# Optimization experiments

Measured on AMD Instinct MI355X. Metric: run time of the kernel, lower is better.

Reference implementation:

```python
import jax, jax.numpy as jnp
import numpy as np

H = 32
W = 32
CIN = 64
GR = 4
CC = 6  # channels_count
N = 2


def build_a(h, w):
    # Faithful replication of the torch buffer construction (incl. overlapping
    # writes into channel 0, which accumulate multiple -1 entries per row).
    num = h * w
    a = np.zeros((num, CC, num), np.float32)
    for i in range(num):
        if (i + 1) % w != 0 and i + 1 < num:
            a[i, 0, i] = 1.0
            a[i, 0, i + 1] = -1.0
        if i + w < num:
            a[i, 1, i] = 1.0
            a[i, 1, i + w] = -1.0
        if (i + 2) % w != 0 and (i + 1) % w != 0 and (i + 2 < num):
            a[i, 2, i] = 1.0
            a[i, 2, i + 2] = -1.0
        if i + 2 * w < num:
            a[i, 3, i] = 1.0
            a[i, 3, i + 2 * w] = -1.0
        if i % w != 0 and i + w < num:
            a[i, 0, i] = 1.0
            a[i, 0, i + w - 1] = -1.0
        if (i + 1) % w != 0 and i + w < num:
            a[i, 0, i] = 1.0
            a[i, 0, i + w + 1] = -1.0
    for k in range(CC):
        a[-1, k, -1] = 1.0
    return jnp.asarray(a)


def conv2d(x, w, b, pad):
    y = jax.lax.conv_general_dilated(
        x, w, window_strides=(1, 1), padding=[(pad, pad), (pad, pad)],
        dimension_numbers=('NCHW', 'OIHW', 'NCHW'))
    return y + b[None, :, None, None]


def setup_inputs() -> dict:
    key = jax.random.key(0)
    ks = jax.random.split(key, 20)
    s = 0.05
    d = {
        'x': jax.random.normal(ks[0], (N, CIN, H, W), jnp.float32),
        'a': build_a(H, W),
        # grad branch: conv3x3 CIN->CIN, conv3x3 CIN->CC*GR
        'gw1': jax.random.normal(ks[1], (CIN, CIN, 3, 3), jnp.float32) * s,
        'gb1': jnp.zeros((CIN,), jnp.float32),
        'gw2': jax.random.normal(ks[2], (CC * GR, CIN, 3, 3), jnp.float32) * s,
        'gb2': jnp.zeros((CC * GR,), jnp.float32),
        # att branch (sigmoid at end)
        'aw1': jax.random.normal(ks[3], (CIN, CIN, 3, 3), jnp.float32) * s,
        'ab1': jnp.zeros((CIN,), jnp.float32),
        'aw2': jax.random.normal(ks[4], (CC * GR, CIN, 3, 3), jnp.float32) * s,
        'ab2': jnp.zeros((CC * GR,), jnp.float32),
        # SE branch: 1x1 CIN->CIN//2, 1x1 CIN//2->GR
        'sw1': jax.random.normal(ks[5], (CIN // 2, CIN, 1, 1), jnp.float32) * s,
        'sb1': jnp.zeros((CIN // 2,), jnp.float32),
        'sw2': jax.random.normal(ks[6], (GR, CIN // 2, 1, 1), jnp.float32) * s,
        'sb2': jnp.zeros((GR,), jnp.float32),
        # GroupNorm(1, GR) affine params
        'gn_g': jnp.ones((GR,), jnp.float32),
        'gn_b': jnp.zeros((GR,), jnp.float32),
        # post conv3x3 GR->128
        'pw': jax.random.normal(ks[7], (128, GR, 3, 3), jnp.float32) * s,
        'pb': jnp.zeros((128,), jnp.float32),
    }
    return d


def reference(x, a, gw1, gb1, gw2, gb2, aw1, ab1, aw2, ab2,
              sw1, sb1, sw2, sb2, gn_g, gn_b, pw, pb):
    n, c, h, w = x.shape
    hw = h * w
    lrelu = lambda t: jax.nn.leaky_relu(t, 0.01)

    att = jax.nn.sigmoid(conv2d(lrelu(conv2d(x, aw1, ab1, 1)), aw2, ab2, 1))
    grad = conv2d(lrelu(conv2d(x, gw1, gb1, 1)), gw2, gb2, 1)
    pooled = jnp.mean(x, axis=(2, 3), keepdims=True)
    se = jax.nn.sigmoid(conv2d(lrelu(conv2d(pooled, sw1, sb1, 0)), sw2, sb2, 0))  # [n,GR,1,1]

    b = n * GR
    att = att.reshape(b, CC, hw, 1).transpose(0, 2, 1, 3)   # [b, hw, CC, 1]
    grad = grad.reshape(b, CC, hw, 1).transpose(0, 2, 1, 3)  # [b, hw, CC, 1]

    A = (a[None] * att).reshape(b, hw * CC, hw)   # [b, hw*CC, hw]
    B = (grad * att).reshape(b, hw * CC)          # [b, hw*CC]

    ATA = jnp.einsum('bkm,bkn->bmn', A, A) + 1e-12 * jnp.eye(hw, dtype=x.dtype)
    ATB = jnp.einsum('bkm,bk->bm', A, B)[..., None]
    sol = jnp.linalg.solve(ATA, ATB).reshape(n, GR, h, w)

    # GroupNorm(1, GR): normalize over all (GR,h,w) per sample, per-channel affine
    mu = jnp.mean(sol, axis=(1, 2, 3), keepdims=True)
    var = jnp.var(sol, axis=(1, 2, 3), keepdims=True)
    y = (sol - mu) / jnp.sqrt(var + 1e-5)
    y = y * gn_g[None, :, None, None] + gn_b[None, :, None, None]

    y = se * y
    return conv2d(y, pw, pb, 1)
```

## Files before the change

### kernel.cpp

```cpp
#include <hip/hip_runtime.h>
#include <math.h>

#define HW 1024

__device__ __forceinline__ float lrelu(float v) { return v > 0.f ? v : 0.01f * v; }
__device__ __forceinline__ float sigmoidf(float v) { return 1.f / (1.f + expf(-v)); }

__device__ __forceinline__ float dpp_prev(float x) {
  return __int_as_float(__builtin_amdgcn_update_dpp(
      0, __float_as_int(x), 0x111, 0xF, 0xF, true));
}
__device__ __forceinline__ float dpp_next(float x) {
  return __int_as_float(__builtin_amdgcn_update_dpp(
      0, __float_as_int(x), 0x101, 0xF, 0xF, true));
}

template <int CTRL, int RMASK>
__device__ __forceinline__ float dpp_add(float x) {
  return x + __int_as_float(__builtin_amdgcn_update_dpp(
      0, __float_as_int(x), CTRL, RMASK, 0xF, true));
}
__device__ __forceinline__ float wave_red_bcast(float x) {
  x = dpp_add<0x111, 0xF>(x);
  x = dpp_add<0x112, 0xF>(x);
  x = dpp_add<0x114, 0xF>(x);
  x = dpp_add<0x118, 0xF>(x);
  x = dpp_add<0x142, 0xA>(x);
  x = dpp_add<0x143, 0xC>(x);
  return __int_as_float(__builtin_amdgcn_readlane(__float_as_int(x), 63));
}

__device__ __forceinline__ float frcp(float x) { return __builtin_amdgcn_rcpf(x); }

__device__ __forceinline__ float block_reduce(float v, float* red, int tid) {
#pragma unroll
  for (int off = 32; off > 0; off >>= 1) v += __shfl_xor(v, off, 64);
  if ((tid & 63) == 0) red[tid >> 6] = v;
  __syncthreads();
  float s = red[0] + red[1] + red[2] + red[3];
  __syncthreads();
  return s;
}

template <int MODE>
__device__ __forceinline__ void conv_direct(
    const float* __restrict__ X,
    const float* __restrict__ Wb,
    float bias,
    float* __restrict__ outp,
    int rb) {
  __shared__ float4 sred[192];
  __shared__ float wl[576];
  int tid = threadIdx.x;
  int w = tid >> 6, l = tid & 63;
  int c4 = l & 7, ry = l >> 3;
  int r = rb * 8 + ry;
  int c0 = c4 * 4;
  float lmf = (c4 == 0) ? 0.f : 1.f;
  float rmf = (c4 == 7) ? 0.f : 1.f;
  if (tid < 144) ((float4*)wl)[tid] = ((const float4*)Wb)[tid];
  int rrc[3];
  float rmk[3];
#pragma unroll
  for (int dr = 0; dr < 3; ++dr) {
    int rr = r - 1 + dr;
    bool ok = (unsigned)rr < 32u;
    rrc[dr] = ok ? rr * 32 : 0;
    rmk[dr] = ok ? 1.f : 0.f;
  }
  __syncthreads();
  const float* Xw = X + w * 16 * HW;
  const float* Wp = wl + w * 144;
  float ax = 0.f, ay = 0.f, az = 0.f, aq = 0.f;
#pragma unroll 4
  for (int i = 0; i < 16; ++i) {
    const float* pl = Xw + i * HW;
    const float* wq = Wp + i * 9;
#pragma unroll
    for (int dr = 0; dr < 3; ++dr) {
      const float* rp = pl + rrc[dr];
      float4 m = *(const float4*)(rp + c0);
      float L = dpp_prev(m.w) * lmf;
      float R = dpp_next(m.x) * rmf;
      float w0 = wq[dr * 3 + 0] * rmk[dr];
      float w1 = wq[dr * 3 + 1] * rmk[dr];
      float w2 = wq[dr * 3 + 2] * rmk[dr];
      ax += w0 * L   + w1 * m.x + w2 * m.y;
      ay += w0 * m.x + w1 * m.y + w2 * m.z;
      az += w0 * m.y + w1 * m.z + w2 * m.w;
      aq += w0 * m.z + w1 * m.w + w2 * R;
    }
  }
  __syncthreads();
  if (w > 0) sred[(w - 1) * 64 + l] = make_float4(ax, ay, az, aq);
  __syncthreads();
  if (w == 0) {
    float4 p0 = sred[l], p1 = sred[64 + l], p2 = sred[128 + l];
    float o0 = ax + p0.x + p1.x + p2.x + bias;
    float o1 = ay + p0.y + p1.y + p2.y + bias;
    float o2 = az + p0.z + p1.z + p2.z + bias;
    float o3 = aq + p0.w + p1.w + p2.w + bias;
    if (MODE == 0) { o0 = lrelu(o0); o1 = lrelu(o1); o2 = lrelu(o2); o3 = lrelu(o3); }
    else if (MODE == 1) { o0 = sigmoidf(o0); o1 = sigmoidf(o1); o2 = sigmoidf(o2); o3 = sigmoidf(o3); }
    *(float4*)(outp + r * 32 + c0) = make_float4(o0, o1, o2, o3);
  }
}

__global__ __launch_bounds__(256) void conv64_pool(const float* __restrict__ x,
    const float* __restrict__ aw, const float* __restrict__ ab,
    const float* __restrict__ gw, const float* __restrict__ gb,
    float* __restrict__ t1, float* __restrict__ pooled) {
  int bx = blockIdx.x;
  if (bx < 1024) {
    int co = bx & 63, t = bx >> 6, rb = t & 3, g = t >> 2;
    int br = g >> 1, n = g & 1;
    conv_direct<0>(x + n * 64 * HW,
                   (br ? gw : aw) + co * 576,
                   (br ? gb : ab)[co],
                   t1 + (g * 64 + co) * HW, rb);
  } else {
    __shared__ float red[4];
    int p = bx - 1024;
    const float* px = x + p * HW;
    int tid = threadIdx.x;
    float s = px[tid] + px[tid + 256] + px[tid + 512] + px[tid + 768];
    s = block_reduce(s, red, tid);
    if (tid == 0) pooled[p] = s * (1.f / 1024.f);
  }
}

__global__ __launch_bounds__(256) void conv24_k(const float* __restrict__ t1,
    const float* __restrict__ aw2, const float* __restrict__ ab2,
    const float* __restrict__ gw2, const float* __restrict__ gb2,
    float* __restrict__ attb, float* __restrict__ gradb) {
  int bx = blockIdx.x;
  int co = bx % 24, t = bx / 24, rb = t & 3, g = t >> 2;
  int br = g >> 1, n = g & 1;
  const float* X = t1 + g * 64 * HW;
  const float* Wb = (br ? gw2 : aw2) + co * 576;
  float bias = (br ? gb2 : ab2)[co];
  float* outp = (br ? gradb : attb) + (n * 24 + co) * HW;
  if (br) conv_direct<2>(X, Wb, bias, outp, rb);
  else    conv_direct<1>(X, Wb, bias, outp, rb);
}

__global__ __launch_bounds__(256, 1) void cg_solve(const float* __restrict__ att,
    const float* __restrict__ grad, float* __restrict__ sol,
    int maxit, float tolrel) {
  int b = blockIdx.x, tid = threadIdx.x;
  __shared__ float As[7 * 1088];
  __shared__ __align__(16) float ub0[1152];
  __shared__ __align__(16) float ub1[1152];
  __shared__ __align__(16) float2 redb[2][4];
  float* OD1  = As;
  float* OD2  = As + 1 * 1088;
  float* OD30 = As + 2 * 1088;
  float* OD31 = As + 3 * 1088;
  float* OD32 = As + 4 * 1088;
  float* OD33 = As + 5 * 1088;
  float* OD64 = As + 6 * 1088;
  for (int i = tid; i < 448; i += 256) As[(i >> 6) * 1088 + (i & 63)] = 0.f;
  if (tid < 64) {
    ub0[tid] = 0.f; ub0[1088 + tid] = 0.f;
    ub1[tid] = 0.f; ub1[1088 + tid] = 0.f;
  }

  const float* attb = att + b * 6 * HW;
  const float* grdb = grad + b * 6 * HW;
  const int m0 = 4 * tid;
  const int idx0 = 64 + m0;
  float rk[4], d0v[4], d0r[4];
#pragma unroll
  for (int k = 0; k < 4; ++k) {
    int m = m0 + k;
    int mr = m & 31;
    bool p1 = (mr != 31) && (m < 1023);
    bool p2 = (mr != 0) && (m < 992);
    bool p3 = (mr != 31) && (m < 992);
    bool dd = p1 | p2 | p3;
    bool c1 = m < 992;
    bool c2 = (mr != 30) && (mr != 31) && (m < 1022);
    bool c3 = m < 960;
    float a0 = attb[m],            g0 = grdb[m];
    float a1 = attb[HW + m],       g1 = grdb[HW + m];
    float a2 = attb[2 * HW + m],   g2 = grdb[2 * HW + m];
    float a3 = attb[3 * HW + m],   g3 = grdb[3 * HW + m];
    float u0 = a0 * a0, t0 = u0 * g0;
    float u1 = a1 * a1, t1 = u1 * g1;
    float u2 = a2 * a2, t2 = u2 * g2;
    float u3 = a3 * a3, t3 = u3 * g3;
    float u0m1 = 0.f, t0m1 = 0.f; bool p1m1 = false, p2m1 = false, p3m1 = false;
    if (m >= 1) {
      int j = m - 1; int jr = j & 31;
      p1m1 = (jr != 31) && (j < 1023); p2m1 = (jr != 0) && (j < 992); p3m1 = (jr != 31) && (j < 992);
      float a = attb[j], g = grdb[j]; u0m1 = a * a; t0m1 = u0m1 * g;
    }
    float u0m31 = 0.f, t0m31 = 0.f; bool p2m31 = false, p3m31 = false;
    if (m >= 31) {
      int j = m - 31; int jr = j & 31;
      p2m31 = (jr != 0) && (j < 992); p3m31 = (jr != 31) && (j < 992);
      float a = attb[j], g = grdb[j]; u0m31 = a * a; t0m31 = u0m31 * g;
    }
    float u0m33 = 0.f, t0m33 = 0.f; bool p3m33 = false;
    if (m >= 33) {
      int j = m - 33; int jr = j & 31;
      p3m33 = (jr != 31) && (j < 992);
      float a = attb[j], g = grdb[j]; u0m33 = a * a; t0m33 = u0m33 * g;
    }
    float u1m32 = 0.f, t1m32 = 0.f; bool c1m32 = false;
    if (m >= 32) {
      int j = m - 32; c1m32 = (j < 992);
      float a = attb[HW + j], g = grdb[HW + j]; u1m32 = a * a; t1m32 = u1m32 * g;
    }
    float u2m2 = 0.f, t2m2 = 0.f; bool c2m2 = false;
    if (m >= 2) {
      int j = m - 2; int jr = j & 31;
      c2m2 = (jr != 30) && (jr != 31) && (j < 1022);
      float a = attb[2 * HW + j], g = grdb[2 * HW + j]; u2m2 = a * a; t2m2 = u2m2 * g;
    }
    float u3m64 = 0.f, t3m64 = 0.f; bool c3m64 = false;
    if (m >= 64) {
      int j = m - 64; c3m64 = (j < 960);
      float a = attb[3 * HW + j], g = grdb[3 * HW + j]; u3m64 = a * a; t3m64 = u3m64 * g;
    }
    float d0 = (dd ? u0 : 0.f) + (c1 ? u1 : 0.f) + (c2 ? u2 : 0.f) + (c3 ? u3 : 0.f)
             + (p1m1 ? u0m1 : 0.f) + (p2m31 ? u0m31 : 0.f) + (p3m33 ? u0m33 : 0.f)
             + (c1m32 ? u1m32 : 0.f) + (c2m2 ? u2m2 : 0.f) + (c3m64 ? u3m64 : 0.f) + 1e-12f;
    float rhs = (dd ? t0 : 0.f) + (c1 ? t1 : 0.f) + (c2 ? t2 : 0.f) + (c3 ? t3 : 0.f)
              - (p1m1 ? t0m1 : 0.f) - (p2m31 ? t0m31 : 0.f) - (p3m33 ? t0m33 : 0.f)
              - (c1m32 ? t1m32 : 0.f) - (c2m2 ? t2m2 : 0.f) - (c3m64 ? t3m64 : 0.f);
    if (m == 1023) {
      float a4 = attb[4 * HW + 1023], g4 = grdb[4 * HW + 1023];
      float a5 = attb[5 * HW + 1023], g5 = grdb[5 * HW + 1023];
      d0 += u0 + u1 + u2 + u3 + a4 * a4 + a5 * a5;
      rhs += t0 + t1 + t2 + t3 + a4 * a4 * g4 + a5 * a5 * g5;
    }
    int idx = idx0 + k;
    OD1[idx]  = p1 ? -u0 : 0.f;
    OD31[idx] = p2 ? -u0 : 0.f;
    OD33[idx] = p3 ? -u0 : 0.f;
    OD2[idx]  = (c2 ? -u2 : 0.f) + ((p2m31 && p3m31) ? u0m31 : 0.f);
    OD30[idx] = (p1m1 && p2m1) ? u0m1 : 0.f;
    OD32[idx] = (c1 ? -u1 : 0.f) + ((p1m1 && p3m1) ? u0m1 : 0.f);
    OD64[idx] = c3 ? -u3 : 0.f;
    d0v[k] = d0;
    d0r[k] = 1.f / d0;
    rk[k] = rhs;
  }
  __syncthreads();

  float c1p[4], c1m[4], c2p[4], c2m[4], c30p[4], c30m[4], c31p[4], c31m[4];
  float c32p[4], c32m[4], c33p[4], c33m[4], c64p[4], c64m[4];
#pragma unroll
  for (int k = 0; k < 4; ++k) {
    int idx = idx0 + k;
    c1p[k]  = OD1[idx];  c1m[k]  = OD1[idx - 1];
    c2p[k]  = OD2[idx];  c2m[k]  = OD2[idx - 2];
    c30p[k] = OD30[idx]; c30m[k] = OD30[idx - 30];
    c31p[k] = OD31[idx]; c31m[k] = OD31[idx - 31];
    c32p[k] = OD32[idx]; c32m[k] = OD32[idx - 32];
    c33p[k] = OD33[idx]; c33m[k] = OD33[idx - 33];
    c64p[k] = OD64[idx]; c64m[k] = OD64[idx - 64];
  }

#define SPMV(BASE, UK, NK)                                                   \
  {                                                                          \
    const float* bp = (BASE) + idx0;                                         \
    float2 A01 = *(const float2*)(bp - 2);                                   \
    float2 A67 = *(const float2*)(bp + 4);                                   \
    float2 B01 = *(const float2*)(bp + 30);                                  \
    float4 B25 = *(const float4*)(bp + 32);                                  \
    float  B6  = bp[36];                                                     \
    float  C0  = bp[-33];                                                    \
    float4 C14 = *(const float4*)(bp - 32);                                  \
    float2 C56 = *(const float2*)(bp - 28);                                  \
    float4 Dp  = *(const float4*)(bp + 64);                                  \
    float4 Ep  = *(const float4*)(bp - 64);                                  \
    float Aa[8] = {A01.x, A01.y, UK[0], UK[1], UK[2], UK[3], A67.x, A67.y};  \
    float Ba[7] = {B01.x, B01.y, B25.x, B25.y, B25.z, B25.w, B6};            \
    float Ca[7] = {C0, C14.x, C14.y, C14.z, C14.w, C56.x, C56.y};            \
    float Da[4] = {Dp.x, Dp.y, Dp.z, Dp.w};                                  \
    float Ea[4] = {Ep.x, Ep.y, Ep.z, Ep.w};                                  \
    _Pragma("unroll")                                                        \
    for (int k = 0; k < 4; ++k) {                                            \
      float v = d0v[k] * UK[k];                                              \
      v += c1p[k]  * Aa[3 + k] + c1m[k]  * Aa[1 + k];                        \
      v += c2p[k]  * Aa[4 + k] + c2m[k]  * Aa[k];                            \
      v += c30p[k] * Ba[k]     + c30m[k] * Ca[3 + k];                        \
      v += c31p[k] * Ba[1 + k] + c31m[k] * Ca[2 + k];                        \
      v += c32p[k] * Ba[2 + k] + c32m[k] * Ca[1 + k];                        \
      v += c33p[k] * Ba[3 + k] + c33m[k] * Ca[k];                            \
      v += c64p[k] * Da[k]     + c64m[k] * Ea[k];                            \
      NK[k] = v;                                                             \
    }                                                                        \
  }

  int lane = tid & 63, wv = tid >> 6;
  float xk[4] = {0.f, 0.f, 0.f, 0.f};
  float uk[4], wk[4], mk[4], nk[4];
  float pk[4] = {0.f, 0.f, 0.f, 0.f};
  float sk[4] = {0.f, 0.f, 0.f, 0.f};
  float qk[4] = {0.f, 0.f, 0.f, 0.f};
  float zk[4] = {0.f, 0.f, 0.f, 0.f};

#pragma unroll
  for (int k = 0; k < 4; ++k) uk[k] = rk[k] * d0r[k];
  *(float4*)(ub0 + idx0) = make_float4(uk[0], uk[1], uk[2], uk[3]);
  __syncthreads();
  SPMV(ub0, uk, wk);

  float gp = 1.f, ap_ = 1.f, stop = 0.f;
  for (int it = 0; it < maxit; ++it) {
    float* bw = (it & 1) ? ub0 : ub1;
    float2* rw = redb[it & 1];
#pragma unroll
    for (int k = 0; k < 4; ++k) mk[k] = wk[k] * d0r[k];
    *(float4*)(bw + idx0) = make_float4(mk[0], mk[1], mk[2], mk[3]);
    float gpart = 0.f, dpart = 0.f;
#pragma unroll
    for (int k = 0; k < 4; ++k) { gpart += rk[k] * uk[k]; dpart += wk[k] * uk[k]; }
    float gsum = wave_red_bcast(gpart);
    float dsum = wave_red_bcast(dpart);
    if (lane == 0) rw[wv] = make_float2(gsum, dsum);
    __syncthreads();
    SPMV(bw, mk, nk);
    float4 ra = *(float4*)&rw[0];
    float4 rb2 = *(float4*)&rw[2];
    float gam = ra.x + ra.z + rb2.x + rb2.z;
    float dlt = ra.y + ra.w + rb2.y + rb2.w;
    float beta, alpha;
    if (it == 0) {
      stop = gam * tolrel;
      if (!(fabsf(dlt) > 0.f)) break;
      beta = 0.f;
      alpha = gam * frcp(dlt);
    } else {
      beta = gam * frcp(gp);
      float denom = dlt - beta * (gam * frcp(ap_));
      if (!(fabsf(denom) > 0.f)) break;
      alpha = gam * frcp(denom);
    }
#pragma unroll
    for (int k = 0; k < 4; ++k) {
      zk[k] = nk[k] + beta * zk[k];
      qk[k] = mk[k] + beta * qk[k];
      sk[k] = wk[k] + beta * sk[k];
      pk[k] = uk[k] + beta * pk[k];
      xk[k] += alpha * pk[k];
      rk[k] -= alpha * sk[k];
      uk[k] -= alpha * qk[k];
      wk[k] -= alpha * zk[k];
    }
    gp = gam; ap_ = alpha;
    if (!(gam > stop)) break;
  }
#pragma unroll
  for (int k = 0; k < 4; ++k) sol[b * HW + m0 + k] = xk[k];
#undef SPMV
}

__global__ __launch_bounds__(256) void gnorm_postconv(
    const float* __restrict__ sol, const float* __restrict__ pooled,
    const float* __restrict__ sw1, const float* __restrict__ sb1,
    const float* __restrict__ sw2, const float* __restrict__ sb2,
    const float* __restrict__ gn_g, const float* __restrict__ gn_b,
    const float* __restrict__ pw, const float* __restrict__ pb,
    float* __restrict__ out) {
  int bx = blockIdx.x;
  int n = bx >> 7, co = bx & 127;
  int tid = threadIdx.x;
  __shared__ __align__(16) float yp[4 * 1024];
  __shared__ float wb[36];
  __shared__ float red[4];
  __shared__ float s1[32];
  __shared__ float seg[4];
  if (tid < 36) wb[tid] = pw[co * 36 + tid];
  const float4* s4 = (const float4*)(sol + n * 4096);
  float4 v4[4];
  float sum = 0.f, ssq = 0.f;
#pragma unroll
  for (int k = 0; k < 4; ++k) {
    float4 t = s4[tid + 256 * k];
    v4[k] = t;
    sum += t.x + t.y + t.z + t.w;
    ssq += t.x * t.x + t.y * t.y + t.z * t.z + t.w * t.w;
  }
  sum = block_reduce(sum, red, tid);
  ssq = block_reduce(ssq, red, tid);
  if (tid < 32) {
    float acc = sb1[tid];
    for (int ci = 0; ci < 64; ++ci) acc += sw1[tid * 64 + ci] * pooled[n * 64 + ci];
    s1[tid] = lrelu(acc);
  }
  __syncthreads();
  if (tid < 4) {
    float acc = sb2[tid];
    for (int j = 0; j < 32; ++j) acc += sw2[tid * 32 + j] * s1[j];
    seg[tid] = sigmoidf(acc);
  }
  __syncthreads();
  float mu = sum * (1.f / 4096.f);
  float var = ssq * (1.f / 4096.f) - mu * mu;
  float inv = rsqrtf(var + 1e-5f);
#pragma unroll
  for (int k = 0; k < 4; ++k) {
    int q = tid + 256 * k;
    int g = q >> 8;
    float sA = inv * gn_g[g] * seg[g];
    float sB = (gn_b[g] - mu * inv * gn_g[g]) * seg[g];
    float4 t = v4[k];
    t.x = t.x * sA + sB;
    t.y = t.y * sA + sB;
    t.z = t.z * sA + sB;
    t.w = t.w * sA + sB;
    ((float4*)yp)[q] = t;
  }
  __syncthreads();
  float bias = pb[co];
  float acc[4] = {bias, bias, bias, bias};
#pragma unroll
  for (int k = 0; k < 4; ++k) {
    int m = tid + 256 * k;
    int yy = m >> 5, xx = m & 31;
#pragma unroll
    for (int g = 0; g < 4; ++g) {
      const float* pl = yp + g * 1024;
      const float* wc = wb + g * 9;
#pragma unroll
      for (int dy = -1; dy <= 1; ++dy) {
        int y2 = yy + dy;
        if ((unsigned)y2 < 32u) {
          const float* row = pl + y2 * 32;
#pragma unroll
          for (int dx = -1; dx <= 1; ++dx) {
            int x2 = xx + dx;
            if ((unsigned)x2 < 32u) acc[k] += row[x2] * wc[(dy + 1) * 3 + dx + 1];
          }
        }
      }
    }
  }
#pragma unroll
  for (int k = 0; k < 4; ++k) out[(n * 128 + co) * HW + tid + 256 * k] = acc[k];
}

extern "C" void kernel_launch(void* const* d_in, const int* in_sizes, int n_in,
                              void* d_out, int out_size, void* d_ws, size_t ws_size,
                              hipStream_t stream) {
  const float* x   = (const float*)d_in[0];
  const float* gw1 = (const float*)d_in[2];
  const float* gb1 = (const float*)d_in[3];
  const float* gw2 = (const float*)d_in[4];
  const float* gb2 = (const float*)d_in[5];
  const float* aw1 = (const float*)d_in[6];
  const float* ab1 = (const float*)d_in[7];
  const float* aw2 = (const float*)d_in[8];
  const float* ab2 = (const float*)d_in[9];
  const float* sw1 = (const float*)d_in[10];
  const float* sb1 = (const float*)d_in[11];
  const float* sw2 = (const float*)d_in[12];
  const float* sb2 = (const float*)d_in[13];
  const float* gng = (const float*)d_in[14];
  const float* gnb = (const float*)d_in[15];
  const float* pw  = (const float*)d_in[16];
  const float* pb  = (const float*)d_in[17];
  float* out = (float*)d_out;
  float* ws = (float*)d_ws;

  float* t1     = out;
  float* attb   = ws;
  float* gradb  = ws + 49152;
  float* pooled = ws + 98304;
  float* solv   = ws + 98432;

  conv64_pool<<<1152, 256, 0, stream>>>(x, aw1, ab1, gw1, gb1, t1, pooled);
  conv24_k<<<384, 256, 0, stream>>>(t1, aw2, ab2, gw2, gb2, attb, gradb);
  cg_solve<<<8, 256, 0, stream>>>(attb, gradb, solv, 400, 1e-5f);
  gnorm_postconv<<<256, 256, 0, stream>>>(solv, pooled, sw1, sb1, sw2, sb2,
                                          gng, gnb, pw, pb, out);
}
```

Baseline: 149.8 us.

## Fuse four kernels into one persistent kernel with atomic grid barriers

Merges the conv, conv, CG-solve and groupnorm/postconv kernels into a single persistent 256-block kernel. Stages are separated by software grid barriers built on a global atomic counter, and shared memory is overlaid through a union. This removes three kernel launch gaps and the tail idle time between dependent launches. In exchange, conv stages now run as grid-stride loops over fewer blocks, a memset is added, and correctness depends on all 256 blocks being co-resident.

```diff
diff --git a/kernel.cpp b/kernel.cpp
--- a/kernel.cpp
+++ b/kernel.cpp
@@ -42,15 +42,30 @@
   return s;
 }
 
+union __align__(16) SMem {
+  struct { float4 sred[192]; float wl[576]; float red[4]; } conv;
+  struct { float As[7 * 1088]; float ub0[1152]; float ub1[1152]; float2 redb[2][4]; } cg;
+  struct { float yp[4096]; float wb[36]; float red[4]; float s1[32]; float seg[4]; } gn;
+};
+
+__device__ __forceinline__ void grid_sync(int* bar, int target) {
+  __syncthreads();
+  if (threadIdx.x == 0) {
+    __hip_atomic_fetch_add(bar, 1, __ATOMIC_ACQ_REL, __HIP_MEMORY_SCOPE_AGENT);
+    while (__hip_atomic_load(bar, __ATOMIC_ACQUIRE, __HIP_MEMORY_SCOPE_AGENT) < target)
+      __builtin_amdgcn_s_sleep(8);
+  }
+  __syncthreads();
+}
+
 template <int MODE>
 __device__ __forceinline__ void conv_direct(
     const float* __restrict__ X,
     const float* __restrict__ Wb,
     float bias,
     float* __restrict__ outp,
-    int rb) {
-  __shared__ float4 sred[192];
-  __shared__ float wl[576];
+    int rb,
+    float4* sred, float* wl) {
   int tid = threadIdx.x;
   int w = tid >> 6, l = tid & 63;
   int c4 = l & 7, ry = l >> 3;
@@ -106,162 +121,167 @@
   }
 }
 
-__global__ __launch_bounds__(256) void conv64_pool(const float* __restrict__ x,
-    const float* __restrict__ aw, const float* __restrict__ ab,
-    const float* __restrict__ gw, const float* __restrict__ gb,
-    float* __restrict__ t1, float* __restrict__ pooled) {
-  int bx = blockIdx.x;
-  if (bx < 1024) {
-    int co = bx & 63, t = bx >> 6, rb = t & 3, g = t >> 2;
-    int br = g >> 1, n = g & 1;
-    conv_direct<0>(x + n * 64 * HW,
-                   (br ? gw : aw) + co * 576,
-                   (br ? gb : ab)[co],
-                   t1 + (g * 64 + co) * HW, rb);
-  } else {
-    __shared__ float red[4];
-    int p = bx - 1024;
-    const float* px = x + p * HW;
-    int tid = threadIdx.x;
-    float s = px[tid] + px[tid + 256] + px[tid + 512] + px[tid + 768];
-    s = block_reduce(s, red, tid);
-    if (tid == 0) pooled[p] = s * (1.f / 1024.f);
-  }
-}
-
-__global__ __launch_bounds__(256) void conv24_k(const float* __restrict__ t1,
+__global__ __launch_bounds__(256) void mega(
+    const float* __restrict__ x,
+    const float* __restrict__ aw1, const float* __restrict__ ab1,
+    const float* __restrict__ gw1, const float* __restrict__ gb1,
     const float* __restrict__ aw2, const float* __restrict__ ab2,
     const float* __restrict__ gw2, const float* __restrict__ gb2,
-    float* __restrict__ attb, float* __restrict__ gradb) {
-  int bx = blockIdx.x;
-  int co = bx % 24, t = bx / 24, rb = t & 3, g = t >> 2;
-  int br = g >> 1, n = g & 1;
-  const float* X = t1 + g * 64 * HW;
-  const float* Wb = (br ? gw2 : aw2) + co * 576;
-  float bias = (br ? gb2 : ab2)[co];
-  float* outp = (br ? gradb : attb) + (n * 24 + co) * HW;
-  if (br) conv_direct<2>(X, Wb, bias, outp, rb);
-  else    conv_direct<1>(X, Wb, bias, outp, rb);
-}
-
-__global__ __launch_bounds__(256, 1) void cg_solve(const float* __restrict__ att,
-    const float* __restrict__ grad, float* __restrict__ sol,
-    int maxit, float tolrel) {
-  int b = blockIdx.x, tid = threadIdx.x;
-  __shared__ float As[7 * 1088];
-  __shared__ __align__(16) float ub0[1152];
-  __shared__ __align__(16) float ub1[1152];
-  __shared__ __align__(16) float2 redb[2][4];
-  float* OD1  = As;
-  float* OD2  = As + 1 * 1088;
-  float* OD30 = As + 2 * 1088;
-  float* OD31 = As + 3 * 1088;
-  float* OD32 = As + 4 * 1088;
-  float* OD33 = As + 5 * 1088;
-  float* OD64 = As + 6 * 1088;
-  for (int i = tid; i < 448; i += 256) As[(i >> 6) * 1088 + (i & 63)] = 0.f;
-  if (tid < 64) {
-    ub0[tid] = 0.f; ub0[1088 + tid] = 0.f;
-    ub1[tid] = 0.f; ub1[1088 + tid] = 0.f;
-  }
-
-  const float* attb = att + b * 6 * HW;
-  const float* grdb = grad + b * 6 * HW;
-  const int m0 = 4 * tid;
-  const int idx0 = 64 + m0;
-  float rk[4], d0v[4], d0r[4];
-#pragma unroll
-  for (int k = 0; k < 4; ++k) {
-    int m = m0 + k;
-    int mr = m & 31;
-    bool p1 = (mr != 31) && (m < 1023);
-    bool p2 = (mr != 0) && (m < 992);
-    bool p3 = (mr != 31) && (m < 992);
-    bool dd = p1 | p2 | p3;
-    bool c1 = m < 992;
-    bool c2 = (mr != 30) && (mr != 31) && (m < 1022);
-    bool c3 = m < 960;
-    float a0 = attb[m],            g0 = grdb[m];
-    float a1 = attb[HW + m],       g1 = grdb[HW + m];
-    float a2 = attb[2 * HW + m],   g2 = grdb[2 * HW + m];
-    float a3 = attb[3 * HW + m],   g3 = grdb[3 * HW + m];
-    float u0 = a0 * a0, t0 = u0 * g0;
-    float u1 = a1 * a1, t1 = u1 * g1;
-    float u2 = a2 * a2, t2 = u2 * g2;
-    float u3 = a3 * a3, t3 = u3 * g3;
-    float u0m1 = 0.f, t0m1 = 0.f; bool p1m1 = false, p2m1 = false, p3m1 = false;
-    if (m >= 1) {
-      int j = m - 1; int jr = j & 31;
-      p1m1 = (jr != 31) && (j < 1023); p2m1 = (jr != 0) && (j < 992); p3m1 = (jr != 31) && (j < 992);
-      float a = attb[j], g = grdb[j]; u0m1 = a * a; t0m1 = u0m1 * g;
-    }
-    float u0m31 = 0.f, t0m31 = 0.f; bool p2m31 = false, p3m31 = false;
-    if (m >= 31) {
-      int j = m - 31; int jr = j & 31;
-      p2m31 = (jr != 0) && (j < 992); p3m31 = (jr != 31) && (j < 992);
-      float a = attb[j], g = grdb[j]; u0m31 = a * a; t0m31 = u0m31 * g;
-    }
-    float u0m33 = 0.f, t0m33 = 0.f; bool p3m33 = false;
-    if (m >= 33) {
-      int j = m - 33; int jr = j & 31;
-      p3m33 = (jr != 31) && (j < 992);
-      float a = attb[j], g = grdb[j]; u0m33 = a * a; t0m33 = u0m33 * g;
-    }
-    float u1m32 = 0.f, t1m32 = 0.f; bool c1m32 = false;
-    if (m >= 32) {
-      int j = m - 32; c1m32 = (j < 992);
-      float a = attb[HW + j], g = grdb[HW + j]; u1m32 = a * a; t1m32 = u1m32 * g;
-    }
-    float u2m2 = 0.f, t2m2 = 0.f; bool c2m2 = false;
-    if (m >= 2) {
-      int j = m - 2; int jr = j & 31;
-      c2m2 = (jr != 30) && (jr != 31) && (j < 1022);
-      float a = attb[2 * HW + j], g = grdb[2 * HW + j]; u2m2 = a * a; t2m2 = u2m2 * g;
-    }
-    float u3m64 = 0.f, t3m64 = 0.f; bool c3m64 = false;
-    if (m >= 64) {
-      int j = m - 64; c3m64 = (j < 960);
-      float a = attb[3 * HW + j], g = grdb[3 * HW + j]; u3m64 = a * a; t3m64 = u3m64 * g;
-    }
-    float d0 = (dd ? u0 : 0.f) + (c1 ? u1 : 0.f) + (c2 ? u2 : 0.f) + (c3 ? u3 : 0.f)
-             + (p1m1 ? u0m1 : 0.f) + (p2m31 ? u0m31 : 0.f) + (p3m33 ? u0m33 : 0.f)
-             + (c1m32 ? u1m32 : 0.f) + (c2m2 ? u2m2 : 0.f) + (c3m64 ? u3m64 : 0.f) + 1e-12f;
-    float rhs = (dd ? t0 : 0.f) + (c1 ? t1 : 0.f) + (c2 ? t2 : 0.f) + (c3 ? t3 : 0.f)
-              - (p1m1 ? t0m1 : 0.f) - (p2m31 ? t0m31 : 0.f) - (p3m33 ? t0m33 : 0.f)
-              - (c1m32 ? t1m32 : 0.f) - (c2m2 ? t2m2 : 0.f) - (c3m64 ? t3m64 : 0.f);
-    if (m == 1023) {
-      float a4 = attb[4 * HW + 1023], g4 = grdb[4 * HW + 1023];
-      float a5 = attb[5 * HW + 1023], g5 = grdb[5 * HW + 1023];
-      d0 += u0 + u1 + u2 + u3 + a4 * a4 + a5 * a5;
-      rhs += t0 + t1 + t2 + t3 + a4 * a4 * g4 + a5 * a5 * g5;
-    }
-    int idx = idx0 + k;
-    OD1[idx]  = p1 ? -u0 : 0.f;
-    OD31[idx] = p2 ? -u0 : 0.f;
-    OD33[idx] = p3 ? -u0 : 0.f;
-    OD2[idx]  = (c2 ? -u2 : 0.f) + ((p2m31 && p3m31) ? u0m31 : 0.f);
-    OD30[idx] = (p1m1 && p2m1) ? u0m1 : 0.f;
-    OD32[idx] = (c1 ? -u1 : 0.f) + ((p1m1 && p3m1) ? u0m1 : 0.f);
-    OD64[idx] = c3 ? -u3 : 0.f;
-    d0v[k] = d0;
-    d0r[k] = 1.f / d0;
-    rk[k] = rhs;
-  }
-  __syncthreads();
-
-  float c1p[4], c1m[4], c2p[4], c2m[4], c30p[4], c30m[4], c31p[4], c31m[4];
-  float c32p[4], c32m[4], c33p[4], c33m[4], c64p[4], c64m[4];
-#pragma unroll
-  for (int k = 0; k < 4; ++k) {
-    int idx = idx0 + k;
-    c1p[k]  = OD1[idx];  c1m[k]  = OD1[idx - 1];
-    c2p[k]  = OD2[idx];  c2m[k]  = OD2[idx - 2];
-    c30p[k] = OD30[idx]; c30m[k] = OD30[idx - 30];
-    c31p[k] = OD31[idx]; c31m[k] = OD31[idx - 31];
-    c32p[k] = OD32[idx]; c32m[k] = OD32[idx - 32];
-    c33p[k] = OD33[idx]; c33m[k] = OD33[idx - 33];
-    c64p[k] = OD64[idx]; c64m[k] = OD64[idx - 64];
-  }
+    const float* __restrict__ sw1, const float* __restrict__ sb1,
+    const float* __restrict__ sw2, const float* __restrict__ sb2,
+    const float* __restrict__ gn_g, const float* __restrict__ gn_b,
+    const float* __restrict__ pw, const float* __restrict__ pb,
+    float* t1out,
+    float* __restrict__ attg, float* __restrict__ grdg,
+    float* __restrict__ pooled, float* __restrict__ solv,
+    int* bar, int maxit, float tolrel) {
+  __shared__ SMem su;
+  int bx = blockIdx.x, tid = threadIdx.x;
+
+  for (int u = bx; u < 1152; u += 256) {
+    if (u < 1024) {
+      int co = u & 63, t = u >> 6, rb = t & 3, g = t >> 2;
+      int br = g >> 1, n = g & 1;
+      conv_direct<0>(x + n * 64 * HW,
+                     (br ? gw1 : aw1) + co * 576,
+                     (br ? gb1 : ab1)[co],
+                     t1out + (g * 64 + co) * HW, rb, su.conv.sred, su.conv.wl);
+    } else {
+      int p = u - 1024;
+      const float* px = x + p * HW;
+      float s = px[tid] + px[tid + 256] + px[tid + 512] + px[tid + 768];
+      s = block_reduce(s, su.conv.red, tid);
+      if (tid == 0) pooled[p] = s * (1.f / 1024.f);
+    }
+  }
+  grid_sync(bar, 256);
+
+  for (int u = bx; u < 384; u += 256) {
+    int co = u % 24, t = u / 24, rb = t & 3, g = t >> 2;
+    int br = g >> 1, n = g & 1;
+    const float* X = t1out + g * 64 * HW;
+    const float* Wb = (br ? gw2 : aw2) + co * 576;
+    float bias = (br ? gb2 : ab2)[co];
+    float* outp = (br ? grdg : attg) + (n * 24 + co) * HW;
+    if (br) conv_direct<2>(X, Wb, bias, outp, rb, su.conv.sred, su.conv.wl);
+    else    conv_direct<1>(X, Wb, bias, outp, rb, su.conv.sred, su.conv.wl);
+  }
+  grid_sync(bar, 512);
+
+  if (bx < 8) {
+    int b = bx;
+    float* OD1  = su.cg.As;
+    float* OD2  = su.cg.As + 1 * 1088;
+    float* OD30 = su.cg.As + 2 * 1088;
+    float* OD31 = su.cg.As + 3 * 1088;
+    float* OD32 = su.cg.As + 4 * 1088;
+    float* OD33 = su.cg.As + 5 * 1088;
+    float* OD64 = su.cg.As + 6 * 1088;
+    float* ub0 = su.cg.ub0;
+    float* ub1 = su.cg.ub1;
+    for (int i = tid; i < 448; i += 256) su.cg.As[(i >> 6) * 1088 + (i & 63)] = 0.f;
+    if (tid < 64) {
+      ub0[tid] = 0.f; ub0[1088 + tid] = 0.f;
+      ub1[tid] = 0.f; ub1[1088 + tid] = 0.f;
+    }
+
+    const float* attb = attg + b * 6 * HW;
+    const float* grdb = grdg + b * 6 * HW;
+    const int m0 = 4 * tid;
+    const int idx0 = 64 + m0;
+    float rk[4], d0v[4], d0r[4];
+#pragma unroll
+    for (int k = 0; k < 4; ++k) {
+      int m = m0 + k;
+      int mr = m & 31;
+      bool p1 = (mr != 31) && (m < 1023);
+      bool p2 = (mr != 0) && (m < 992);
+      bool p3 = (mr != 31) && (m < 992);
+      bool dd = p1 | p2 | p3;
+      bool c1 = m < 992;
+      bool c2 = (mr != 30) && (mr != 31) && (m < 1022);
+      bool c3 = m < 960;
+      float a0 = attb[m],            g0 = grdb[m];
+      float a1 = attb[HW + m],       g1 = grdb[HW + m];
+      float a2 = attb[2 * HW + m],   g2 = grdb[2 * HW + m];
+      float a3 = attb[3 * HW + m],   g3 = grdb[3 * HW + m];
+      float u0 = a0 * a0, t0 = u0 * g0;
+      float u1 = a1 * a1, t1 = u1 * g1;
+      float u2 = a2 * a2, t2 = u2 * g2;
+      float u3 = a3 * a3, t3 = u3 * g3;
+      float u0m1 = 0.f, t0m1 = 0.f; bool p1m1 = false, p2m1 = false, p3m1 = false;
+      if (m >= 1) {
+        int j = m - 1; int jr = j & 31;
+        p1m1 = (jr != 31) && (j < 1023); p2m1 = (jr != 0) && (j < 992); p3m1 = (jr != 31) && (j < 992);
+        float a = attb[j], g = grdb[j]; u0m1 = a * a; t0m1 = u0m1 * g;
+      }
+      float u0m31 = 0.f, t0m31 = 0.f; bool p2m31 = false, p3m31 = false;
+      if (m >= 31) {
+        int j = m - 31; int jr = j & 31;
+        p2m31 = (jr != 0) && (j < 992); p3m31 = (jr != 31) && (j < 992);
+        float a = attb[j], g = grdb[j]; u0m31 = a * a; t0m31 = u0m31 * g;
+      }
+      float u0m33 = 0.f, t0m33 = 0.f; bool p3m33 = false;
+      if (m >= 33) {
+        int j = m - 33; int jr = j & 31;
+        p3m33 = (jr != 31) && (j < 992);
+        float a = attb[j], g = grdb[j]; u0m33 = a * a; t0m33 = u0m33 * g;
+      }
+      float u1m32 = 0.f, t1m32 = 0.f; bool c1m32 = false;
+      if (m >= 32) {
+        int j = m - 32; c1m32 = (j < 992);
+        float a = attb[HW + j], g = grdb[HW + j]; u1m32 = a * a; t1m32 = u1m32 * g;
+      }
+      float u2m2 = 0.f, t2m2 = 0.f; bool c2m2 = false;
+      if (m >= 2) {
+        int j = m - 2; int jr = j & 31;
+        c2m2 = (jr != 30) && (jr != 31) && (j < 1022);
+        float a = attb[2 * HW + j], g = grdb[2 * HW + j]; u2m2 = a * a; t2m2 = u2m2 * g;
+      }
+      float u3m64 = 0.f, t3m64 = 0.f; bool c3m64 = false;
+      if (m >= 64) {
+        int j = m - 64; c3m64 = (j < 960);
+        float a = attb[3 * HW + j], g = grdb[3 * HW + j]; u3m64 = a * a; t3m64 = u3m64 * g;
+      }
+      float d0 = (dd ? u0 : 0.f) + (c1 ? u1 : 0.f) + (c2 ? u2 : 0.f) + (c3 ? u3 : 0.f)
+               + (p1m1 ? u0m1 : 0.f) + (p2m31 ? u0m31 : 0.f) + (p3m33 ? u0m33 : 0.f)
+               + (c1m32 ? u1m32 : 0.f) + (c2m2 ? u2m2 : 0.f) + (c3m64 ? u3m64 : 0.f) + 1e-12f;
+      float rhs = (dd ? t0 : 0.f) + (c1 ? t1 : 0.f) + (c2 ? t2 : 0.f) + (c3 ? t3 : 0.f)
+                - (p1m1 ? t0m1 : 0.f) - (p2m31 ? t0m31 : 0.f) - (p3m33 ? t0m33 : 0.f)
+                - (c1m32 ? t1m32 : 0.f) - (c2m2 ? t2m2 : 0.f) - (c3m64 ? t3m64 : 0.f);
+      if (m == 1023) {
+        float a4 = attb[4 * HW + 1023], g4 = grdb[4 * HW + 1023];
+        float a5 = attb[5 * HW + 1023], g5 = grdb[5 * HW + 1023];
+        d0 += u0 + u1 + u2 + u3 + a4 * a4 + a5 * a5;
+        rhs += t0 + t1 + t2 + t3 + a4 * a4 * g4 + a5 * a5 * g5;
+      }
+      int idx = idx0 + k;
+      OD1[idx]  = p1 ? -u0 : 0.f;
+      OD31[idx] = p2 ? -u0 : 0.f;
+      OD33[idx] = p3 ? -u0 : 0.f;
+      OD2[idx]  = (c2 ? -u2 : 0.f) + ((p2m31 && p3m31) ? u0m31 : 0.f);
+      OD30[idx] = (p1m1 && p2m1) ? u0m1 : 0.f;
+      OD32[idx] = (c1 ? -u1 : 0.f) + ((p1m1 && p3m1) ? u0m1 : 0.f);
+      OD64[idx] = c3 ? -u3 : 0.f;
+      d0v[k] = d0;
+      d0r[k] = 1.f / d0;
+      rk[k] = rhs;
+    }
+    __syncthreads();
+
+    float c1p[4], c1m[4], c2p[4], c2m[4], c30p[4], c30m[4], c31p[4], c31m[4];
+    float c32p[4], c32m[4], c33p[4], c33m[4], c64p[4], c64m[4];
+#pragma unroll
+    for (int k = 0; k < 4; ++k) {
+      int idx = idx0 + k;
+      c1p[k]  = OD1[idx];  c1m[k]  = OD1[idx - 1];
+      c2p[k]  = OD2[idx];  c2m[k]  = OD2[idx - 2];
+      c30p[k] = OD30[idx]; c30m[k] = OD30[idx - 30];
+      c31p[k] = OD31[idx]; c31m[k] = OD31[idx - 31];
+      c32p[k] = OD32[idx]; c32m[k] = OD32[idx - 32];
+      c33p[k] = OD33[idx]; c33m[k] = OD33[idx - 33];
+      c64p[k] = OD64[idx]; c64m[k] = OD64[idx - 64];
+    }
 
 #define SPMV(BASE, UK, NK)                                                   \
   {                                                                          \
@@ -295,153 +315,142 @@
     }                                                                        \
   }
 
-  int lane = tid & 63, wv = tid >> 6;
-  float xk[4] = {0.f, 0.f, 0.f, 0.f};
-  float uk[4], wk[4], mk[4], nk[4];
-  float pk[4] = {0.f, 0.f, 0.f, 0.f};
-  float sk[4] = {0.f, 0.f, 0.f, 0.f};
-  float qk[4] = {0.f, 0.f, 0.f, 0.f};
-  float zk[4] = {0.f, 0.f, 0.f, 0.f};
-
-#pragma unroll
-  for (int k = 0; k < 4; ++k) uk[k] = rk[k] * d0r[k];
-  *(float4*)(ub0 + idx0) = make_float4(uk[0], uk[1], uk[2], uk[3]);
-  __syncthreads();
-  SPMV(ub0, uk, wk);
-
-  float gp = 1.f, ap_ = 1.f, stop = 0.f;
-  for (int it = 0; it < maxit; ++it) {
-    float* bw = (it & 1) ? ub0 : ub1;
-    float2* rw = redb[it & 1];
-#pragma unroll
-    for (int k = 0; k < 4; ++k) mk[k] = wk[k] * d0r[k];
-    *(float4*)(bw + idx0) = make_float4(mk[0], mk[1], mk[2], mk[3]);
-    float gpart = 0.f, dpart = 0.f;
-#pragma unroll
-    for (int k = 0; k < 4; ++k) { gpart += rk[k] * uk[k]; dpart += wk[k] * uk[k]; }
-    float gsum = wave_red_bcast(gpart);
-    float dsum = wave_red_bcast(dpart);
-    if (lane == 0) rw[wv] = make_float2(gsum, dsum);
+    int lane = tid & 63, wv = tid >> 6;
+    float xk[4] = {0.f, 0.f, 0.f, 0.f};
+    float uk[4], wk[4], mk[4], nk[4];
+    float pk[4] = {0.f, 0.f, 0.f, 0.f};
+    float sk[4] = {0.f, 0.f, 0.f, 0.f};
+    float qk[4] = {0.f, 0.f, 0.f, 0.f};
+    float zk[4] = {0.f, 0.f, 0.f, 0.f};
+
+#pragma unroll
+    for (int k = 0; k < 4; ++k) uk[k] = rk[k] * d0r[k];
+    *(float4*)(ub0 + idx0) = make_float4(uk[0], uk[1], uk[2], uk[3]);
     __syncthreads();
-    SPMV(bw, mk, nk);
-    float4 ra = *(float4*)&rw[0];
-    float4 rb2 = *(float4*)&rw[2];
-    float gam = ra.x + ra.z + rb2.x + rb2.z;
-    float dlt = ra.y + ra.w + rb2.y + rb2.w;
-    float beta, alpha;
-    if (it == 0) {
-      stop = gam * tolrel;
-      if (!(fabsf(dlt) > 0.f)) break;
-      beta = 0.f;
-      alpha = gam * frcp(dlt);
-    } else {
-      beta = gam * frcp(gp);
-      float denom = dlt - beta * (gam * frcp(ap_));
-      if (!(fabsf(denom) > 0.f)) break;
-      alpha = gam * frcp(denom);
-    }
+    SPMV(ub0, uk, wk);
+
+    float gp = 1.f, ap_ = 1.f, stop = 0.f;
+    for (int it = 0; it < maxit; ++it) {
+      float* bw = (it & 1) ? ub0 : ub1;
+      float2* rw = su.cg.redb[it & 1];
+#pragma unroll
+      for (int k = 0; k < 4; ++k) mk[k] = wk[k] * d0r[k];
+      *(float4*)(bw + idx0) = make_float4(mk[0], mk[1], mk[2], mk[3]);
+      float gpart = 0.f, dpart = 0.f;
+#pragma unroll
+      for (int k = 0; k < 4; ++k) { gpart += rk[k] * uk[k]; dpart += wk[k] * uk[k]; }
+      float gsum = wave_red_bcast(gpart);
+      float dsum = wave_red_bcast(dpart);
+      if (lane == 0) rw[wv] = make_float2(gsum, dsum);
+      __syncthreads();
+      SPMV(bw, mk, nk);
+      float4 ra = *(float4*)&rw[0];
+      float4 rb2 = *(float4*)&rw[2];
+      float gam = ra.x + ra.z + rb2.x + rb2.z;
+      float dlt = ra.y + ra.w + rb2.y + rb2.w;
+      float beta, alpha;
+      if (it == 0) {
+        stop = gam * tolrel;
+        if (!(fabsf(dlt) > 0.f)) break;
+        beta = 0.f;
+        alpha = gam * frcp(dlt);
+      } else {
+        beta = gam * frcp(gp);
+        float denom = dlt - beta * (gam * frcp(ap_));
+        if (!(fabsf(denom) > 0.f)) break;
+        alpha = gam * frcp(denom);
+      }
+#pragma unroll
+      for (int k = 0; k < 4; ++k) {
+        zk[k] = nk[k] + beta * zk[k];
+        qk[k] = mk[k] + beta * qk[k];
+        sk[k] = wk[k] + beta * sk[k];
+        pk[k] = uk[k] + beta * pk[k];
+        xk[k] += alpha * pk[k];
+        rk[k] -= alpha * sk[k];
+        uk[k] -= alpha * qk[k];
+        wk[k] -= alpha * zk[k];
+      }
+      gp = gam; ap_ = alpha;
+      if (!(gam > stop)) break;
+    }
+#pragma unroll
+    for (int k = 0; k < 4; ++k) solv[b * HW + m0 + k] = xk[k];
+#undef SPMV
+  }
+  grid_sync(bar, 768);
+
+  {
+    int n = bx >> 7, co = bx & 127;
+    if (tid < 36) su.gn.wb[tid] = pw[co * 36 + tid];
+    const float4* s4 = (const float4*)(solv + n * 4096);
+    float4 v4[4];
+    float sum = 0.f, ssq = 0.f;
 #pragma unroll
     for (int k = 0; k < 4; ++k) {
-      zk[k] = nk[k] + beta * zk[k];
-      qk[k] = mk[k] + beta * qk[k];
-      sk[k] = wk[k] + beta * sk[k];
-      pk[k] = uk[k] + beta * pk[k];
-      xk[k] += alpha * pk[k];
-      rk[k] -= alpha * sk[k];
-      uk[k] -= alpha * qk[k];
-      wk[k] -= alpha * zk[k];
-    }
-    gp = gam; ap_ = alpha;
-    if (!(gam > stop)) break;
-  }
-#pragma unroll
-  for (int k = 0; k < 4; ++k) sol[b * HW + m0 + k] = xk[k];
-#undef SPMV
-}
-
-__global__ __launch_bounds__(256) void gnorm_postconv(
-    const float* __restrict__ sol, const float* __restrict__ pooled,
-    const float* __restrict__ sw1, const float* __restrict__ sb1,
-    const float* __restrict__ sw2, const float* __restrict__ sb2,
-    const float* __restrict__ gn_g, const float* __restrict__ gn_b,
-    const float* __restrict__ pw, const float* __restrict__ pb,
-    float* __restrict__ out) {
-  int bx = blockIdx.x;
-  int n = bx >> 7, co = bx & 127;
-  int tid = threadIdx.x;
-  __shared__ __align__(16) float yp[4 * 1024];
-  __shared__ float wb[36];
-  __shared__ float red[4];
-  __shared__ float s1[32];
-  __shared__ float seg[4];
-  if (tid < 36) wb[tid] = pw[co * 36 + tid];
-  const float4* s4 = (const float4*)(sol + n * 4096);
-  float4 v4[4];
-  float sum = 0.f, ssq = 0.f;
-#pragma unroll
-  for (int k = 0; k < 4; ++k) {
-    float4 t = s4[tid + 256 * k];
-    v4[k] = t;
-    sum += t.x + t.y + t.z + t.w;
-    ssq += t.x * t.x + t.y * t.y + t.z * t.z + t.w * t.w;
-  }
-  sum = block_reduce(sum, red, tid);
-  ssq = block_reduce(ssq, red, tid);
-  if (tid < 32) {
-    float acc = sb1[tid];
-    for (int ci = 0; ci < 64; ++ci) acc += sw1[tid * 64 + ci] * pooled[n * 64 + ci];
-    s1[tid] = lrelu(acc);
-  }
-  __syncthreads();
-  if (tid < 4) {
-    float acc = sb2[tid];
-    for (int j = 0; j < 32; ++j) acc += sw2[tid * 32 + j] * s1[j];
-    seg[tid] = sigmoidf(acc);
-  }
-  __syncthreads();
-  float mu = sum * (1.f / 4096.f);
-  float var = ssq * (1.f / 4096.f) - mu * mu;
-  float inv = rsqrtf(var + 1e-5f);
-#pragma unroll
-  for (int k = 0; k < 4; ++k) {
-    int q = tid + 256 * k;
-    int g = q >> 8;
-    float sA = inv * gn_g[g] * seg[g];
-    float sB = (gn_b[g] - mu * inv * gn_g[g]) * seg[g];
-    float4 t = v4[k];
-    t.x = t.x * sA + sB;
-    t.y = t.y * sA + sB;
-    t.z = t.z * sA + sB;
-    t.w = t.w * sA + sB;
-    ((float4*)yp)[q] = t;
-  }
-  __syncthreads();
-  float bias = pb[co];
-  float acc[4] = {bias, bias, bias, bias};
-#pragma unroll
-  for (int k = 0; k < 4; ++k) {
-    int m = tid + 256 * k;
-    int yy = m >> 5, xx = m & 31;
-#pragma unroll
-    for (int g = 0; g < 4; ++g) {
-      const float* pl = yp + g * 1024;
-      const float* wc = wb + g * 9;
-#pragma unroll
-      for (int dy = -1; dy <= 1; ++dy) {
-        int y2 = yy + dy;
-        if ((unsigned)y2 < 32u) {
-          const float* row = pl + y2 * 32;
-#pragma unroll
-          for (int dx = -1; dx <= 1; ++dx) {
-            int x2 = xx + dx;
-            if ((unsigned)x2 < 32u) acc[k] += row[x2] * wc[(dy + 1) * 3 + dx + 1];
+      float4 t = s4[tid + 256 * k];
+      v4[k] = t;
+      sum += t.x + t.y + t.z + t.w;
+      ssq += t.x * t.x + t.y * t.y + t.z * t.z + t.w * t.w;
+    }
+    sum = block_reduce(sum, su.gn.red, tid);
+    ssq = block_reduce(ssq, su.gn.red, tid);
+    if (tid < 32) {
+      float acc = sb1[tid];
+      for (int ci = 0; ci < 64; ++ci) acc += sw1[tid * 64 + ci] * pooled[n * 64 + ci];
+      su.gn.s1[tid] = lrelu(acc);
+    }
+    __syncthreads();
+    if (tid < 4) {
+      float acc = sb2[tid];
+      for (int j = 0; j < 32; ++j) acc += sw2[tid * 32 + j] * su.gn.s1[j];
+      su.gn.seg[tid] = sigmoidf(acc);
+    }
+    __syncthreads();
+    float mu = sum * (1.f / 4096.f);
+    float var = ssq * (1.f / 4096.f) - mu * mu;
+    float inv = rsqrtf(var + 1e-5f);
+#pragma unroll
+    for (int k = 0; k < 4; ++k) {
+      int q = tid + 256 * k;
+      int g = q >> 8;
+      float sA = inv * gn_g[g] * su.gn.seg[g];
+      float sB = (gn_b[g] - mu * inv * gn_g[g]) * su.gn.seg[g];
+      float4 t = v4[k];
+      t.x = t.x * sA + sB;
+      t.y = t.y * sA + sB;
+      t.z = t.z * sA + sB;
+      t.w = t.w * sA + sB;
+      ((float4*)su.gn.yp)[q] = t;
+    }
+    __syncthreads();
+    float bias = pb[co];
+    float acc[4] = {bias, bias, bias, bias};
+#pragma unroll
+    for (int k = 0; k < 4; ++k) {
+      int m = tid + 256 * k;
+      int yy = m >> 5, xx = m & 31;
+#pragma unroll
+      for (int g = 0; g < 4; ++g) {
+        const float* pl = su.gn.yp + g * 1024;
+        const float* wc = su.gn.wb + g * 9;
+#pragma unroll
+        for (int dy = -1; dy <= 1; ++dy) {
+          int y2 = yy + dy;
+          if ((unsigned)y2 < 32u) {
+            const float* row = pl + y2 * 32;
+#pragma unroll
+            for (int dx = -1; dx <= 1; ++dx) {
+              int x2 = xx + dx;
+              if ((unsigned)x2 < 32u) acc[k] += row[x2] * wc[(dy + 1) * 3 + dx + 1];
+            }
           }
         }
       }
     }
-  }
-#pragma unroll
-  for (int k = 0; k < 4; ++k) out[(n * 128 + co) * HW + tid + 256 * k] = acc[k];
+#pragma unroll
+    for (int k = 0; k < 4; ++k) t1out[(n * 128 + co) * HW + tid + 256 * k] = acc[k];
+  }
 }
 
 extern "C" void kernel_launch(void* const* d_in, const int* in_sizes, int n_in,
@@ -467,15 +476,15 @@
   float* out = (float*)d_out;
   float* ws = (float*)d_ws;
 
-  float* t1     = out;
   float* attb   = ws;
   float* gradb  = ws + 49152;
   float* pooled = ws + 98304;
   float* solv   = ws + 98432;
-
-  conv64_pool<<<1152, 256, 0, stream>>>(x, aw1, ab1, gw1, gb1, t1, pooled);
-  conv24_k<<<384, 256, 0, stream>>>(t1, aw2, ab2, gw2, gb2, attb, gradb);
-  cg_solve<<<8, 256, 0, stream>>>(attb, gradb, solv, 400, 1e-5f);
-  gnorm_postconv<<<256, 256, 0, stream>>>(solv, pooled, sw1, sb1, sw2, sb2,
-                                          gng, gnb, pw, pb, out);
-}
+  int*   bar    = (int*)(ws + 106624);
+
+  hipMemsetAsync(bar, 0, 64, stream);
+  mega<<<256, 256, 0, stream>>>(x, aw1, ab1, gw1, gb1, aw2, ab2, gw2, gb2,
+                                sw1, sb1, sw2, sb2, gng, gnb, pw, pb,
+                                out, attb, gradb, pooled, solv,
+                                bar, 400, 1e-5f);
+}
```

Result: slower. 228.0 us (+52.2%).
